# Performance work log

Measured on AMD Instinct MI355X. Metric: run time of the kernel, lower is better.

Reference implementation:

```python
import jax, jax.numpy as jnp
import numpy as np

N_NODES = 50000
KEEP_PROB = 0.5  # dropout = 0.5


def setup_inputs() -> dict:
    key = jax.random.key(0)
    k1, k2, k3, k4, k5 = jax.random.split(key, 5)
    S, E, DIN, DOUT = 2, 800000, 512, 128
    x = jax.random.normal(k1, (N_NODES, DIN), dtype=jnp.float32)
    weights = jax.random.normal(k2, (S, DIN, DOUT), dtype=jnp.float32) * (1.0 / np.sqrt(DIN))
    adj_rows = jax.random.randint(k3, (S, E), 0, N_NODES, dtype=jnp.int32)
    adj_cols = jax.random.randint(k4, (S, E), 0, N_NODES, dtype=jnp.int32)
    adj_vals = jax.random.uniform(k5, (S, E), dtype=jnp.float32)
    return {"x": x, "weights": weights, "adj_rows": adj_rows,
            "adj_cols": adj_cols, "adj_vals": adj_vals}


def reference(x, weights, adj_rows, adj_cols, adj_vals):
    # Dropout (TF semantics: mask and scale by 1/keep_prob), fixed key for determinism.
    mask = (jax.random.uniform(jax.random.key(42), x.shape) < KEEP_PROB)
    xd = x * mask.astype(x.dtype) / KEEP_PROB
    # Dense GEMM per support: pre_sup[s] = dropout(x) @ W_s  -> [S, N, Dout]
    pre_sup = jnp.einsum('nd,sdo->sno', xd, weights)
    # SpMM per support: out[s] = A_s @ pre_sup[s] with A_s in COO form.
    def spmm(rows, cols, vals, h):
        return jax.ops.segment_sum(vals[:, None] * h[cols], rows,
                                   num_segments=N_NODES)
    out = jax.vmap(spmm)(adj_rows, adj_cols, adj_vals, pre_sup)  # [S, N, Dout]
    return jax.nn.relu(out)
```

## Files before the change

kernel.cpp:

```cpp
#include <hip/hip_runtime.h>
#include <stdint.h>

#define N_NODES 50000
#define DIN     512
#define DOUT    128
#define NSUP    2
#define EDGES   800000
#define NEDGE   (NSUP * EDGES)
#define NROWS   (NSUP * N_NODES)
#define NB      782
#define CH      8192
#define NCH     ((NEDGE + CH - 1) / CH)
#define EPT     16
#define SCAP    4096
#define NMASKW  ((N_NODES * DIN) / 32)

typedef __attribute__((ext_vector_type(8))) short short8;
typedef __attribute__((ext_vector_type(4))) float f32x4;

__device__ __forceinline__ uint32_t rotl32(uint32_t v, uint32_t d) {
  return (v << d) | (v >> (32u - d));
}

__device__ __forceinline__ void threefry2x32(uint32_t x0, uint32_t x1,
                                             uint32_t& o0, uint32_t& o1) {
  const uint32_t ks0 = 0u;
  const uint32_t ks1 = 42u;
  const uint32_t ks2 = 0u ^ 42u ^ 0x1BD11BDAu;
  x0 += ks0; x1 += ks1;
#define TF_R(r) { x0 += x1; x1 = rotl32(x1, (r)); x1 ^= x0; }
  TF_R(13) TF_R(15) TF_R(26) TF_R(6)
  x0 += ks1; x1 += ks2 + 1u;
  TF_R(17) TF_R(29) TF_R(16) TF_R(24)
  x0 += ks2; x1 += ks0 + 2u;
  TF_R(13) TF_R(15) TF_R(26) TF_R(6)
  x0 += ks0; x1 += ks1 + 3u;
  TF_R(17) TF_R(29) TF_R(16) TF_R(24)
  x0 += ks1; x1 += ks2 + 4u;
  TF_R(13) TF_R(15) TF_R(26) TF_R(6)
  x0 += ks2; x1 += ks0 + 5u;
#undef TF_R
  o0 = x0; o1 = x1;
}

__device__ __forceinline__ bool keep_mask(uint32_t idx) {
  uint32_t o0, o1;
  threefry2x32(0u, idx, o0, o1);
  uint32_t bits = o0 ^ o1;
  float u = __uint_as_float((bits >> 9) | 0x3F800000u) - 1.0f;
  return u < 0.5f;
}

__device__ __forceinline__ uint32_t pack_bf16x2(float a, float b) {
  uint32_t ua = __float_as_uint(a), ub = __float_as_uint(b);
  ua += 0x7fffu + ((ua >> 16) & 1u);
  ub += 0x7fffu + ((ub >> 16) & 1u);
  return (ua >> 16) | (ub & 0xffff0000u);
}

__device__ __forceinline__ uint32_t bf16rne(float f) {
  uint32_t u = __float_as_uint(f);
  u += 0x7fffu + ((u >> 16) & 1u);
  return u >> 16;
}

__global__ __launch_bounds__(256) void maskgen(uint32_t* __restrict__ maskbuf) {
  int wid = blockIdx.x * 256 + threadIdx.x;
  if (wid >= NMASKW) return;
  uint32_t base = (uint32_t)wid * 32u;
  uint32_t m = 0u;
#pragma unroll 4
  for (int q = 0; q < 32; ++q)
    m |= (keep_mask(base + q) ? 1u : 0u) << q;
  maskbuf[wid] = m;
}

__global__ __launch_bounds__(256) void wcvt(const float* __restrict__ w,
                                            unsigned short* __restrict__ b16t) {
  int i = blockIdx.x * 256 + threadIdx.x;
  if (i >= NSUP * DIN * DOUT) return;
  int s   = i >> 16;
  int rem = i & 65535;
  int k   = rem >> 7;
  int o   = rem & 127;
  b16t[(size_t)(s * DOUT + o) * DIN + k] = (unsigned short)bf16rne(w[i]);
}

__global__ __launch_bounds__(512) void gemm_mfma2(
    const float* __restrict__ x, const uint32_t* __restrict__ maskbuf,
    const unsigned short* __restrict__ b16t,
    unsigned short* __restrict__ pre16) {
  __shared__ unsigned short As[128 * 64];
  __shared__ unsigned short Bs[256 * 64];
  const int t    = threadIdx.x;
  const int lane = t & 63;
  const int w    = t >> 6;
  const int wr   = w >> 2;
  const int wc   = w & 3;
  const int m0   = blockIdx.x * 128;

  f32x4 acc[4][4];
#pragma unroll
  for (int i = 0; i < 4; ++i)
#pragma unroll
    for (int j = 0; j < 4; ++j) acc[i][j] = (f32x4){0.f, 0.f, 0.f, 0.f};

  for (int kc = 0; kc < DIN; kc += 64) {
    __syncthreads();
#pragma unroll
    for (int i = 0; i < 2; ++i) {
      int slot = i * 512 + t;
      int row  = slot >> 3;
      int k8   = (slot & 7) * 8;
      int grow = m0 + row;
      union { uint32_t u[4]; short8 s; } pk;
      if (grow < N_NODES) {
        uint32_t b8 = (uint32_t)grow * DIN + (uint32_t)(kc + k8);
        const float4* src = reinterpret_cast<const float4*>(x + b8);
        float4 v0 = src[0], v1 = src[1];
        float f[8] = {v0.x, v0.y, v0.z, v0.w, v1.x, v1.y, v1.z, v1.w};
        uint32_t bits = maskbuf[b8 >> 5] >> (b8 & 31u);
#pragma unroll
        for (int q = 0; q < 8; ++q)
          f[q] = ((bits >> q) & 1u) ? f[q] * 2.0f : 0.0f;
#pragma unroll
        for (int q = 0; q < 4; ++q) pk.u[q] = pack_bf16x2(f[2 * q], f[2 * q + 1]);
      } else {
#pragma unroll
        for (int q = 0; q < 4; ++q) pk.u[q] = 0u;
      }
      *reinterpret_cast<short8*>(&As[(row * 64 + k8) ^ ((row & 7) << 3)]) = pk.s;
    }
#pragma unroll
    for (int i = 0; i < 4; ++i) {
      int slot = i * 512 + t;
      int col  = slot >> 3;
      int k8   = (slot & 7) * 8;
      short8 v = *reinterpret_cast<const short8*>(
          b16t + (size_t)col * DIN + kc + k8);
      *reinterpret_cast<short8*>(&Bs[(col * 64 + k8) ^ ((col & 7) << 3)]) = v;
    }
    __syncthreads();

    short8 af[4][2], bf[2][4];
#pragma unroll
    for (int mf = 0; mf < 4; ++mf)
#pragma unroll
      for (int kk = 0; kk < 2; ++kk) {
        int row = wr * 64 + mf * 16 + (lane & 15);
        int idx = (row * 64 + kk * 32 + (lane >> 4) * 8) ^ ((row & 7) << 3);
        af[mf][kk] = *reinterpret_cast<const short8*>(&As[idx]);
      }
#pragma unroll
    for (int kk = 0; kk < 2; ++kk)
#pragma unroll
      for (int nf = 0; nf < 4; ++nf) {
        int col = wc * 64 + nf * 16 + (lane & 15);
        int idx = (col * 64 + kk * 32 + (lane >> 4) * 8) ^ ((col & 7) << 3);
        bf[kk][nf] = *reinterpret_cast<const short8*>(&Bs[idx]);
      }
#pragma unroll
    for (int mf = 0; mf < 4; ++mf)
#pragma unroll
      for (int nf = 0; nf < 4; ++nf)
#pragma unroll
        for (int kk = 0; kk < 2; ++kk)
          acc[mf][nf] = __builtin_amdgcn_mfma_f32_16x16x32_bf16(
              af[mf][kk], bf[kk][nf], acc[mf][nf], 0, 0, 0);
  }

#pragma unroll
  for (int mf = 0; mf < 4; ++mf) {
    int rbase = m0 + wr * 64 + mf * 16 + ((lane >> 4) * 4);
#pragma unroll
    for (int nf = 0; nf < 4; ++nf) {
      int col = wc * 64 + nf * 16 + (lane & 15);
      int s = col >> 7, o = col & 127;
#pragma unroll
      for (int q = 0; q < 4; ++q) {
        int row = rbase + q;
        if (row < N_NODES)
          pre16[(size_t)(s * N_NODES + row) * DOUT + o] =
              (unsigned short)bf16rne(acc[mf][nf][q]);
      }
    }
  }
}

__global__ __launch_bounds__(512) void count_b(const int* __restrict__ rows,
                                               int* __restrict__ gcnt) {
  __shared__ int hist[NB];
  int t = threadIdx.x;
  for (int b = t; b < NB; b += 512) hist[b] = 0;
  __syncthreads();
  int e0 = blockIdx.x * CH;
#pragma unroll
  for (int i = 0; i < EPT; ++i) {
    int e = e0 + i * 512 + t;
    if (e < NEDGE) {
      int s = (e >= EDGES) ? 1 : 0;
      int grow = s * N_NODES + rows[e];
      atomicAdd(&hist[grow >> 7], 1);
    }
  }
  __syncthreads();
  for (int b = t; b < NB; b += 512)
    if (hist[b]) atomicAdd(&gcnt[b], hist[b]);
}

__global__ __launch_bounds__(1024) void scan782(const int* __restrict__ gcnt,
                                                int* __restrict__ bstart,
                                                int* __restrict__ gcursor) {
  __shared__ int sm[1024];
  int t = threadIdx.x;
  int c = (t < NB) ? gcnt[t] : 0;
  sm[t] = c;
  __syncthreads();
  for (int d = 1; d < 1024; d <<= 1) {
    int v = sm[t];
    int a = (t >= d) ? sm[t - d] : 0;
    __syncthreads();
    sm[t] = v + a;
    __syncthreads();
  }
  if (t < NB) {
    int ex = sm[t] - c;
    bstart[t] = ex;
    gcursor[t] = ex;
  }
  if (t == NB - 1) bstart[NB] = sm[t];
}

__global__ __launch_bounds__(512) void bin_scatter(
    const int* __restrict__ rows, const int* __restrict__ cols,
    const float* __restrict__ vals, int* __restrict__ gcursor,
    uint64_t* __restrict__ binned) {
  __shared__ uint32_t hist[NB];
  __shared__ uint32_t hexcl[NB];
  __shared__ uint32_t sbase[NB];
  __shared__ uint32_t scanb[512];
  __shared__ uint64_t ordered[CH];
  __shared__ uint16_t bk16[CH];
  int t = threadIdx.x;
  for (int b = t; b < NB; b += 512) hist[b] = 0;
  __syncthreads();
  int e0 = blockIdx.x * CH;
  uint32_t key[EPT], rank[EPT], bkt[EPT], vbits[EPT];
#pragma unroll
  for (int i = 0; i < EPT; ++i) {
    int e = e0 + i * 512 + t;
    if (e < NEDGE) {
      int s = (e >= EDGES) ? 1 : 0;
      uint32_t grow = (uint32_t)(s * N_NODES + rows[e]);
      uint32_t gcol = (uint32_t)(s * N_NODES + cols[e]);
      vbits[i] = __float_as_uint(vals[e]);
      uint32_t b = grow >> 7;
      bkt[i] = b;
      key[i] = ((grow & 127u) << 17) | gcol;
      rank[i] = atomicAdd(&hist[b], 1u);
    } else {
      bkt[i] = 0xFFFFFFFFu;
    }
  }
  __syncthreads();
  int t2 = t * 2;
  uint32_t a0 = (t2 < NB) ? hist[t2] : 0u;
  uint32_t a1 = (t2 + 1 < NB) ? hist[t2 + 1] : 0u;
  scanb[t] = a0 + a1;
  __syncthreads();
  for (int d = 1; d < 512; d <<= 1) {
    uint32_t v = scanb[t];
    uint32_t a = (t >= d) ? scanb[t - d] : 0u;
    __syncthreads();
    scanb[t] = v + a;
    __syncthreads();
  }
  uint32_t base  = t ? scanb[t - 1] : 0u;
  uint32_t total = scanb[511];
  if (t2 < NB)     hexcl[t2]     = base;
  if (t2 + 1 < NB) hexcl[t2 + 1] = base + a0;
  for (int b = t; b < NB; b += 512)
    if (hist[b]) sbase[b] = (uint32_t)atomicAdd(&gcursor[b], (int)hist[b]);
  __syncthreads();
#pragma unroll
  for (int i = 0; i < EPT; ++i) {
    if (bkt[i] != 0xFFFFFFFFu) {
      uint32_t slot = hexcl[bkt[i]] + rank[i];
      ordered[slot] = ((uint64_t)vbits[i] << 32) | key[i];
      bk16[slot] = (uint16_t)bkt[i];
    }
  }
  __syncthreads();
#pragma unroll
  for (int i = 0; i < EPT; ++i) {
    uint32_t slot = (uint32_t)(i * 512 + t);
    if (slot < total) {
      uint32_t b = bk16[slot];
      uint32_t dst = sbase[b] + (slot - hexcl[b]);
      binned[dst] = ordered[slot];
    }
  }
}

__global__ __launch_bounds__(512) void sort_bucket(
    const int* __restrict__ bstart, uint64_t* __restrict__ binned,
    int* __restrict__ row_start) {
  __shared__ uint64_t ordered[SCAP];
  __shared__ uint32_t hist[128];
  __shared__ uint32_t excl[128];
  const int t = threadIdx.x;
  const int b = blockIdx.x;
  const int beg = bstart[b], end = bstart[b + 1];
  const int cnt = end - beg;
  if (t < 128) hist[t] = 0;
  __syncthreads();
  uint64_t ed[8];
  uint32_t rk[8], rw[8];
#pragma unroll
  for (int i = 0; i < 8; ++i) {
    int slot = i * 512 + t;
    if (slot < cnt) {
      uint64_t e = binned[beg + slot];
      ed[i] = e;
      uint32_t rowin = ((uint32_t)e >> 17) & 127u;
      rw[i] = rowin;
      rk[i] = atomicAdd(&hist[rowin], 1u);
    } else {
      rw[i] = 0xFFFFFFFFu;
    }
  }
  __syncthreads();
  if (t < 128) excl[t] = hist[t];
  __syncthreads();
  for (int d = 1; d < 128; d <<= 1) {
    uint32_t v = (t < 128) ? excl[t] : 0u;
    uint32_t a = (t >= d && t < 128) ? excl[t - d] : 0u;
    __syncthreads();
    if (t < 128) excl[t] = v + a;
    __syncthreads();
  }
  if (t < 128) {
    uint32_t ex = excl[t] - hist[t];
    int grow = b * 128 + t;
    if (grow < NROWS) row_start[grow] = beg + (int)ex;
    excl[t] = ex;
  }
  __syncthreads();
#pragma unroll
  for (int i = 0; i < 8; ++i)
    if (rw[i] != 0xFFFFFFFFu)
      ordered[excl[rw[i]] + rk[i]] = ed[i];
  __syncthreads();
#pragma unroll
  for (int i = 0; i < 8; ++i) {
    int slot = i * 512 + t;
    if (slot < cnt) binned[beg + slot] = ordered[slot];
  }
  if (b == 0 && t == 0) row_start[NROWS] = NEDGE;
}

__global__ __launch_bounds__(256) void spmm_pull(
    const int* __restrict__ row_start, const uint64_t* __restrict__ binned,
    const uint32_t* __restrict__ preu, float* __restrict__ out) {
  int rid  = blockIdx.x * 4 + (threadIdx.x >> 6);
  int lane = threadIdx.x & 63;
  if (rid >= NROWS) return;
  int beg = row_start[rid];
  int end = row_start[rid + 1];
  float a0 = 0.f, a1 = 0.f;
  int j = beg;
  for (; j + 4 <= end; j += 4) {
    uint64_t e0 = binned[j],     e1 = binned[j + 1];
    uint64_t e2 = binned[j + 2], e3 = binned[j + 3];
    uint32_t q0 = preu[(size_t)((uint32_t)e0 & 0x1FFFFu) * 64 + lane];
    uint32_t q1 = preu[(size_t)((uint32_t)e1 & 0x1FFFFu) * 64 + lane];
    uint32_t q2 = preu[(size_t)((uint32_t)e2 & 0x1FFFFu) * 64 + lane];
    uint32_t q3 = preu[(size_t)((uint32_t)e3 & 0x1FFFFu) * 64 + lane];
    float v0 = __uint_as_float((uint32_t)(e0 >> 32));
    float v1 = __uint_as_float((uint32_t)(e1 >> 32));
    float v2 = __uint_as_float((uint32_t)(e2 >> 32));
    float v3 = __uint_as_float((uint32_t)(e3 >> 32));
    a0 += v0 * __uint_as_float(q0 << 16);
    a1 += v0 * __uint_as_float(q0 & 0xffff0000u);
    a0 += v1 * __uint_as_float(q1 << 16);
    a1 += v1 * __uint_as_float(q1 & 0xffff0000u);
    a0 += v2 * __uint_as_float(q2 << 16);
    a1 += v2 * __uint_as_float(q2 & 0xffff0000u);
    a0 += v3 * __uint_as_float(q3 << 16);
    a1 += v3 * __uint_as_float(q3 & 0xffff0000u);
  }
  for (; j < end; ++j) {
    uint64_t e = binned[j];
    uint32_t q = preu[(size_t)((uint32_t)e & 0x1FFFFu) * 64 + lane];
    float v = __uint_as_float((uint32_t)(e >> 32));
    a0 += v * __uint_as_float(q << 16);
    a1 += v * __uint_as_float(q & 0xffff0000u);
  }
  float2 o = make_float2(fmaxf(a0, 0.f), fmaxf(a1, 0.f));
  *reinterpret_cast<float2*>(out + (size_t)rid * DOUT + 2 * lane) = o;
}

extern "C" void kernel_launch(void* const* d_in, const int* in_sizes, int n_in,
                              void* d_out, int out_size, void* d_ws, size_t ws_size,
                              hipStream_t stream) {
  const float* x    = (const float*)d_in[0];
  const float* w    = (const float*)d_in[1];
  const int*   rows = (const int*)d_in[2];
  const int*   cols = (const int*)d_in[3];
  const float* vals = (const float*)d_in[4];
  float* out = (float*)d_out;

  uint32_t* base = (uint32_t*)d_ws;
  uint32_t* preu       = base;
  unsigned short* b16t = (unsigned short*)(base + 6400000);
  uint32_t* maskbuf    = base + 6400000 + 65536;
  int* gcnt      = (int*)(base + 6400000 + 65536 + 800000);
  int* bstart    = gcnt + 800;
  int* gcursor   = bstart + 800;
  int* row_start = gcursor + 800;
  uint64_t* binned = (uint64_t*)(row_start + 100004);
  size_t need = ((size_t)6400000 + 65536 + 800000 + 2400 + 100004 + 3200000) * 4;
  if (ws_size < need) return;

  hipMemsetAsync(gcnt, 0, NB * sizeof(int), stream);

  maskgen<<<(NMASKW + 255) / 256, 256, 0, stream>>>(maskbuf);
  wcvt<<<(NSUP * DIN * DOUT + 255) / 256, 256, 0, stream>>>(w, b16t);

  gemm_mfma2<<<(N_NODES + 127) / 128, 512, 0, stream>>>(x, maskbuf, b16t,
                                                        (unsigned short*)preu);

  count_b<<<NCH, 512, 0, stream>>>(rows, gcnt);
  scan782<<<1, 1024, 0, stream>>>(gcnt, bstart, gcursor);
  bin_scatter<<<NCH, 512, 0, stream>>>(rows, cols, vals, gcursor, binned);
  sort_bucket<<<NB, 512, 0, stream>>>(bstart, binned, row_start);

  spmm_pull<<<(NROWS + 3) / 4, 256, 0, stream>>>(row_start, binned, preu, out);
}
```

Baseline: 216.8 us.

## Fuse mask generation with edge counting and bucket sort with SpMM pull

Merges dropout mask generation into the edge-histogram kernel and fuses the per-bucket sort into the SpMM gather, so rows are accumulated directly from the shared-memory ordered buffer. This removes the row_start array, the write-back of sorted edges to global memory, and two kernel launches. The keep test is also simplified to a single top-bit check, which is equivalent for keep probability 0.5. In exchange, the SpMM now runs with only 782 blocks of 8 waves, each looping over 16 rows, which lowers parallelism and latency hiding for the gather.

Result: faster. 208.3 us (-3.9%).

```diff
diff --git a/kernel.cpp b/kernel.cpp
--- a/kernel.cpp
+++ b/kernel.cpp
@@ -47,8 +47,7 @@
   uint32_t o0, o1;
   threefry2x32(0u, idx, o0, o1);
   uint32_t bits = o0 ^ o1;
-  float u = __uint_as_float((bits >> 9) | 0x3F800000u) - 1.0f;
-  return u < 0.5f;
+  return (bits >> 31) == 0u;
 }
 
 __device__ __forceinline__ uint32_t pack_bf16x2(float a, float b) {
@@ -64,15 +63,40 @@
   return u >> 16;
 }
 
-__global__ __launch_bounds__(256) void maskgen(uint32_t* __restrict__ maskbuf) {
-  int wid = blockIdx.x * 256 + threadIdx.x;
-  if (wid >= NMASKW) return;
-  uint32_t base = (uint32_t)wid * 32u;
-  uint32_t m = 0u;
+__global__ __launch_bounds__(512) void count_mask(
+    const int* __restrict__ rows, int* __restrict__ gcnt,
+    uint32_t* __restrict__ maskbuf) {
+  const int t = threadIdx.x;
+  const int gtid = blockIdx.x * 512 + t;
+#pragma unroll
+  for (int q = 0; q < 2; ++q) {
+    int wid = gtid * 2 + q;
+    if (wid < NMASKW) {
+      uint32_t base = (uint32_t)wid * 32u;
+      uint32_t m = 0u;
 #pragma unroll 4
-  for (int q = 0; q < 32; ++q)
-    m |= (keep_mask(base + q) ? 1u : 0u) << q;
-  maskbuf[wid] = m;
+      for (int j = 0; j < 32; ++j)
+        m |= (keep_mask(base + j) ? 1u : 0u) << j;
+      maskbuf[wid] = m;
+    }
+  }
+  if (blockIdx.x >= NCH) return;
+  __shared__ int hist[NB];
+  for (int b = t; b < NB; b += 512) hist[b] = 0;
+  __syncthreads();
+  int e0 = blockIdx.x * CH;
+#pragma unroll
+  for (int i = 0; i < EPT; ++i) {
+    int e = e0 + i * 512 + t;
+    if (e < NEDGE) {
+      int s = (e >= EDGES) ? 1 : 0;
+      int grow = s * N_NODES + rows[e];
+      atomicAdd(&hist[grow >> 7], 1);
+    }
+  }
+  __syncthreads();
+  for (int b = t; b < NB; b += 512)
+    if (hist[b]) atomicAdd(&gcnt[b], hist[b]);
 }
 
 __global__ __launch_bounds__(256) void wcvt(const float* __restrict__ w,
@@ -185,27 +209,6 @@
       }
     }
   }
-}
-
-__global__ __launch_bounds__(512) void count_b(const int* __restrict__ rows,
-                                               int* __restrict__ gcnt) {
-  __shared__ int hist[NB];
-  int t = threadIdx.x;
-  for (int b = t; b < NB; b += 512) hist[b] = 0;
-  __syncthreads();
-  int e0 = blockIdx.x * CH;
-#pragma unroll
-  for (int i = 0; i < EPT; ++i) {
-    int e = e0 + i * 512 + t;
-    if (e < NEDGE) {
-      int s = (e >= EDGES) ? 1 : 0;
-      int grow = s * N_NODES + rows[e];
-      atomicAdd(&hist[grow >> 7], 1);
-    }
-  }
-  __syncthreads();
-  for (int b = t; b < NB; b += 512)
-    if (hist[b]) atomicAdd(&gcnt[b], hist[b]);
 }
 
 __global__ __launch_bounds__(1024) void scan782(const int* __restrict__ gcnt,
@@ -302,9 +305,9 @@
   }
 }
 
-__global__ __launch_bounds__(512) void sort_bucket(
-    const int* __restrict__ bstart, uint64_t* __restrict__ binned,
-    int* __restrict__ row_start) {
+__global__ __launch_bounds__(512) void spmm_sort_pull(
+    const int* __restrict__ bstart, const uint64_t* __restrict__ binned,
+    const uint32_t* __restrict__ preu, float* __restrict__ out) {
   __shared__ uint64_t ordered[SCAP];
   __shared__ uint32_t hist[128];
   __shared__ uint32_t excl[128];
@@ -339,65 +342,53 @@
     if (t < 128) excl[t] = v + a;
     __syncthreads();
   }
-  if (t < 128) {
-    uint32_t ex = excl[t] - hist[t];
-    int grow = b * 128 + t;
-    if (grow < NROWS) row_start[grow] = beg + (int)ex;
-    excl[t] = ex;
-  }
+  if (t < 128) excl[t] -= hist[t];
   __syncthreads();
 #pragma unroll
   for (int i = 0; i < 8; ++i)
     if (rw[i] != 0xFFFFFFFFu)
       ordered[excl[rw[i]] + rk[i]] = ed[i];
   __syncthreads();
-#pragma unroll
-  for (int i = 0; i < 8; ++i) {
-    int slot = i * 512 + t;
-    if (slot < cnt) binned[beg + slot] = ordered[slot];
-  }
-  if (b == 0 && t == 0) row_start[NROWS] = NEDGE;
-}
-
-__global__ __launch_bounds__(256) void spmm_pull(
-    const int* __restrict__ row_start, const uint64_t* __restrict__ binned,
-    const uint32_t* __restrict__ preu, float* __restrict__ out) {
-  int rid  = blockIdx.x * 4 + (threadIdx.x >> 6);
-  int lane = threadIdx.x & 63;
-  if (rid >= NROWS) return;
-  int beg = row_start[rid];
-  int end = row_start[rid + 1];
-  float a0 = 0.f, a1 = 0.f;
-  int j = beg;
-  for (; j + 4 <= end; j += 4) {
-    uint64_t e0 = binned[j],     e1 = binned[j + 1];
-    uint64_t e2 = binned[j + 2], e3 = binned[j + 3];
-    uint32_t q0 = preu[(size_t)((uint32_t)e0 & 0x1FFFFu) * 64 + lane];
-    uint32_t q1 = preu[(size_t)((uint32_t)e1 & 0x1FFFFu) * 64 + lane];
-    uint32_t q2 = preu[(size_t)((uint32_t)e2 & 0x1FFFFu) * 64 + lane];
-    uint32_t q3 = preu[(size_t)((uint32_t)e3 & 0x1FFFFu) * 64 + lane];
-    float v0 = __uint_as_float((uint32_t)(e0 >> 32));
-    float v1 = __uint_as_float((uint32_t)(e1 >> 32));
-    float v2 = __uint_as_float((uint32_t)(e2 >> 32));
-    float v3 = __uint_as_float((uint32_t)(e3 >> 32));
-    a0 += v0 * __uint_as_float(q0 << 16);
-    a1 += v0 * __uint_as_float(q0 & 0xffff0000u);
-    a0 += v1 * __uint_as_float(q1 << 16);
-    a1 += v1 * __uint_as_float(q1 & 0xffff0000u);
-    a0 += v2 * __uint_as_float(q2 << 16);
-    a1 += v2 * __uint_as_float(q2 & 0xffff0000u);
-    a0 += v3 * __uint_as_float(q3 << 16);
-    a1 += v3 * __uint_as_float(q3 & 0xffff0000u);
-  }
-  for (; j < end; ++j) {
-    uint64_t e = binned[j];
-    uint32_t q = preu[(size_t)((uint32_t)e & 0x1FFFFu) * 64 + lane];
-    float v = __uint_as_float((uint32_t)(e >> 32));
-    a0 += v * __uint_as_float(q << 16);
-    a1 += v * __uint_as_float(q & 0xffff0000u);
-  }
-  float2 o = make_float2(fmaxf(a0, 0.f), fmaxf(a1, 0.f));
-  *reinterpret_cast<float2*>(out + (size_t)rid * DOUT + 2 * lane) = o;
+
+  const int lane = t & 63, wave = t >> 6;
+  for (int r8 = 0; r8 < 16; ++r8) {
+    int r = wave * 16 + r8;
+    int grow = b * 128 + r;
+    if (grow >= NROWS) break;
+    int jbeg = excl[r];
+    int jend = jbeg + (int)hist[r];
+    float a0 = 0.f, a1 = 0.f;
+    int j = jbeg;
+    for (; j + 4 <= jend; j += 4) {
+      uint64_t e0 = ordered[j],     e1 = ordered[j + 1];
+      uint64_t e2 = ordered[j + 2], e3 = ordered[j + 3];
+      uint32_t q0 = preu[(size_t)((uint32_t)e0 & 0x1FFFFu) * 64 + lane];
+      uint32_t q1 = preu[(size_t)((uint32_t)e1 & 0x1FFFFu) * 64 + lane];
+      uint32_t q2 = preu[(size_t)((uint32_t)e2 & 0x1FFFFu) * 64 + lane];
+      uint32_t q3 = preu[(size_t)((uint32_t)e3 & 0x1FFFFu) * 64 + lane];
+      float v0 = __uint_as_float((uint32_t)(e0 >> 32));
+      float v1 = __uint_as_float((uint32_t)(e1 >> 32));
+      float v2 = __uint_as_float((uint32_t)(e2 >> 32));
+      float v3 = __uint_as_float((uint32_t)(e3 >> 32));
+      a0 += v0 * __uint_as_float(q0 << 16);
+      a1 += v0 * __uint_as_float(q0 & 0xffff0000u);
+      a0 += v1 * __uint_as_float(q1 << 16);
+      a1 += v1 * __uint_as_float(q1 & 0xffff0000u);
+      a0 += v2 * __uint_as_float(q2 << 16);
+      a1 += v2 * __uint_as_float(q2 & 0xffff0000u);
+      a0 += v3 * __uint_as_float(q3 << 16);
+      a1 += v3 * __uint_as_float(q3 & 0xffff0000u);
+    }
+    for (; j < jend; ++j) {
+      uint64_t e = ordered[j];
+      uint32_t q = preu[(size_t)((uint32_t)e & 0x1FFFFu) * 64 + lane];
+      float v = __uint_as_float((uint32_t)(e >> 32));
+      a0 += v * __uint_as_float(q << 16);
+      a1 += v * __uint_as_float(q & 0xffff0000u);
+    }
+    float2 o = make_float2(fmaxf(a0, 0.f), fmaxf(a1, 0.f));
+    *reinterpret_cast<float2*>(out + (size_t)grow * DOUT + 2 * lane) = o;
+  }
 }
 
 extern "C" void kernel_launch(void* const* d_in, const int* in_sizes, int n_in,
@@ -417,23 +408,19 @@
   int* gcnt      = (int*)(base + 6400000 + 65536 + 800000);
   int* bstart    = gcnt + 800;
   int* gcursor   = bstart + 800;
-  int* row_start = gcursor + 800;
-  uint64_t* binned = (uint64_t*)(row_start + 100004);
-  size_t need = ((size_t)6400000 + 65536 + 800000 + 2400 + 100004 + 3200000) * 4;
+  uint64_t* binned = (uint64_t*)(gcursor + 800);
+  size_t need = ((size_t)6400000 + 65536 + 800000 + 2400 + 3200000) * 4;
   if (ws_size < need) return;
 
   hipMemsetAsync(gcnt, 0, NB * sizeof(int), stream);
 
-  maskgen<<<(NMASKW + 255) / 256, 256, 0, stream>>>(maskbuf);
+  count_mask<<<800, 512, 0, stream>>>(rows, gcnt, maskbuf);
+  scan782<<<1, 1024, 0, stream>>>(gcnt, bstart, gcursor);
+  bin_scatter<<<NCH, 512, 0, stream>>>(rows, cols, vals, gcursor, binned);
+
   wcvt<<<(NSUP * DIN * DOUT + 255) / 256, 256, 0, stream>>>(w, b16t);
-
   gemm_mfma2<<<(N_NODES + 127) / 128, 512, 0, stream>>>(x, maskbuf, b16t,
                                                         (unsigned short*)preu);
 
-  count_b<<<NCH, 512, 0, stream>>>(rows, gcnt);
-  scan782<<<1, 1024, 0, stream>>>(gcnt, bstart, gcursor);
-  bin_scatter<<<NCH, 512, 0, stream>>>(rows, cols, vals, gcursor, binned);
-  sort_bucket<<<NB, 512, 0, stream>>>(bstart, binned, row_start);
-
-  spmm_pull<<<(NROWS + 3) / 4, 256, 0, stream>>>(row_start, binned, preu, out);
-}
+  spmm_sort_pull<<<NB, 512, 0, stream>>>(bstart, binned, preu, out);
+}
```
